# Kernel optimization log

Measured on AMD Instinct MI355X. Metric: run time of the kernel, lower is better.

## Reference

```python
import jax, jax.numpy as jnp
import numpy as np

BN_EPS = 1e-5

def _tok2img(f):
    # f: [197, 768] tokens (CLS first). Drop CLS, transpose, reshape -> [1, 768, 14, 14].
    # fv4[0, c, i, j] = f[1 + i*14 + j, c], identical to the original triple loop.
    return f[1:].T.reshape(1, 768, 14, 14)

def _resize(x, s):
    # PyTorch F.interpolate(mode='bilinear', align_corners=False) == jax.image.resize 'bilinear'
    n, c, h, w = x.shape
    return jax.image.resize(x, (n, c, h * s, w * s), method='bilinear')

def _conv_relu_bn(x, conv_w, conv_b, g, b, m, v):
    y = jax.lax.conv_general_dilated(x, conv_w, window_strides=(1, 1), padding='SAME',
                                     dimension_numbers=('NCHW', 'OIHW', 'NCHW'))
    y = y + conv_b[None, :, None, None]
    y = jax.nn.relu(y)
    # BatchNorm2d(1) in eval mode with running stats
    scale = g * jax.lax.rsqrt(v + BN_EPS)
    return y * scale[None, :, None, None] + (b - m * scale)[None, :, None, None]

def setup_inputs() -> dict:
    key = jax.random.key(0)
    ks = jax.random.split(key, 4)
    return {
        'x': jax.random.normal(ks[0], (14, 14), dtype=jnp.float32),
        'fv': jax.random.normal(ks[1], (4, 197, 768), dtype=jnp.float32),
        'conv_w': jax.random.normal(ks[2], (1, 769, 3, 3), dtype=jnp.float32) * 0.02,
        'conv_b': jnp.zeros((1,), jnp.float32),
        'bn_gamma': jnp.ones((1,), jnp.float32),
        'bn_beta': jnp.zeros((1,), jnp.float32),
        'bn_mean': jnp.zeros((1,), jnp.float32),
        'bn_var': jnp.ones((1,), jnp.float32),
        'W_w': jax.random.normal(ks[3], (224, 224), dtype=jnp.float32) * 0.05,
        'W_b': jnp.zeros((224,), jnp.float32),
    }

def reference(x, fv, conv_w, conv_b, bn_gamma, bn_beta, bn_mean, bn_var, W_w, W_b):
    h = x[None, None]  # [1,1,14,14]
    # skip features, pre-resized to match current resolution at each stage
    feats = (
        _tok2img(fv[3]),              # 14x14
        _resize(_tok2img(fv[2]), 2),  # 28x28
        _resize(_tok2img(fv[1]), 4),  # 56x56
        _resize(_tok2img(fv[0]), 8),  # 112x112
    )
    for f in feats:
        h = jnp.concatenate([h, f], axis=1)  # [1,769,H,W]
        h = _conv_relu_bn(h, conv_w, conv_b, bn_gamma, bn_beta, bn_mean, bn_var)
        h = _resize(h, 2)
    # Linear(224,224) over the last dim of [1,1,224,224]
    h = jnp.einsum('nchw,ow->ncho', h, W_w) + W_b
    return jax.nn.sigmoid(h)
```

## Files before the change

kernel.cpp:

```cpp
#include <hip/hip_runtime.h>
#include <math.h>


#define BN_EPS 1e-5f

__device__ __forceinline__ float clampf(float x, float lo, float hi) {
    return fminf(fmaxf(x, lo), hi);
}

__device__ __forceinline__ void srcRange(int dlo, int dhi, int srcH, int& slo, int& shi) {
    int H = 2 * srcH;
    int p0 = max(dlo - 1, 0), p1 = min(dhi + 1, H - 1);
    float h0 = fmaxf(((float)p0 + 0.5f) * 0.5f - 0.5f, 0.f);
    float h1 = fmaxf(((float)p1 + 0.5f) * 0.5f - 0.5f, 0.f);
    slo = (int)h0;
    shi = min((int)h1 + 1, srcH - 1);
}

__device__ __forceinline__ void bRange(int dlo, int dhi, int H, int& lo, int& hi) {
    float sc = 14.f / (float)H;
    int p0 = max(dlo - 1, 0), p1 = min(dhi + 1, H - 1);
    float f0 = clampf(((float)p0 + 0.5f) * sc - 0.5f, 0.f, 13.f);
    float f1 = clampf(((float)p1 + 0.5f) * sc - 0.5f, 0.f, 13.f);
    lo = (int)f0;
    hi = min((int)f1 + 1, 13);
}

__constant__ int kW[4] = {14, 28, 56, 112};
__constant__ int kG[4] = {0, 1764, 5292, 12348};

__global__ __launch_bounds__(1024)
void compute_B_kernel(const float* __restrict__ fv, const float* __restrict__ conv_w,
                      const float* __restrict__ W_w,
                      float* __restrict__ gBt, float* __restrict__ gWTf) {
    __shared__ float part[1008];
    __shared__ float sbrow[126];

    int b = blockIdx.x;
    int s = b / 14, u = b % 14;
    int tid = threadIdx.x;

    if (tid < 448) {
        int idx = b * 448 + tid;
        int o = idx % 224, xx = idx / 224;
        float acc = 0.f;
#pragma unroll
        for (int d = -1; d <= 2; ++d) {
            int w = 2 * xx + d;
            if (w < 0 || w > 223) continue;
            float hx = clampf(((float)w + 0.5f) * 0.5f - 0.5f, 0.f, 111.f);
            int xx0 = (int)hx; float fx = hx - (float)xx0; int xx1 = min(xx0 + 1, 111);
            float c = (xx0 == xx ? 1.f - fx : 0.f) + (xx1 == xx ? fx : 0.f);
            acc += c * W_w[o * 224 + w];
        }
        gWTf[xx * 224 + o] = acc;
    }

    if (tid < 1008) {
        int p = tid / 72, r = tid % 72;
        int sl = r / 9, t = r % 9;
        const float* fvrow = fv + ((size_t)(3 - s) * 197 + 1 + u * 14 + p) * 768 + sl * 96;
        const float* cwp = conv_w + (size_t)(1 + sl * 96) * 9 + t;
        float acc = 0.f;
#pragma unroll 32
        for (int m = 0; m < 96; ++m)
            acc += fvrow[m] * cwp[m * 9];
        part[(p * 9 + t) * 8 + sl] = acc;
    }
    __syncthreads();

    if (tid < 126) {
        float v = 0.f;
        int base = tid * 8;
#pragma unroll
        for (int k = 0; k < 8; ++k) v += part[base + k];
        sbrow[tid] = v;
    }
    __syncthreads();

    int W = kW[s], G = kG[s];
    int n = 9 * W;
    if (tid < n) {
        int t = tid / W, q = tid % W;
        float sc = 14.f / (float)W;
        float fx = clampf(((float)q + 0.5f) * sc - 0.5f, 0.f, 13.f);
        int x0 = (int)fx; float f = fx - (float)x0; int x1 = min(x0 + 1, 13);
        float val = (1.f - f) * sbrow[x0 * 9 + t] + f * sbrow[x1 * 9 + t];
        gBt[G + (t * 14 + u) * W + q] = val;
    }
}

__device__ __forceinline__ float stage_px(int i, int j, int H, int srcH,
                                          const float* __restrict__ hsrc, int srcLo,
                                          const float* __restrict__ cB, int nr, int bLo,
                                          const float* __restrict__ cw, float bias) {
    float featScale = 14.f / (float)H;
    float srcMax = (float)(srcH - 1);
    float acc = bias;
#pragma unroll
    for (int a = 0; a < 3; ++a) {
        int p = i + a - 1;
        if (p < 0 || p >= H) continue;
        float fy = clampf(((float)p + 0.5f) * featScale - 0.5f, 0.f, 13.f);
        int by0 = (int)fy; float byf = fy - (float)by0; int by1 = min(by0 + 1, 13);
        const float* b0 = cB + (by0 - bLo) * H;
        const float* b1 = cB + (by1 - bLo) * H;
        float hy = clampf(((float)p + 0.5f) * 0.5f - 0.5f, 0.f, srcMax);
        int hy0 = (int)hy; float fhy = hy - (float)hy0; int hy1 = min(hy0 + 1, srcH - 1);
        const float* h0 = hsrc + (hy0 - srcLo) * srcH;
        const float* h1 = hsrc + (hy1 - srcLo) * srcH;
#pragma unroll
        for (int bq = 0; bq < 3; ++bq) {
            int q = j + bq - 1;
            if (q < 0 || q >= H) continue;
            int t = a * 3 + bq;
            int toff = t * nr * H;
            float bv = (1.f - byf) * b0[toff + q] + byf * b1[toff + q];
            float hx = clampf(((float)q + 0.5f) * 0.5f - 0.5f, 0.f, srcMax);
            int hx0 = (int)hx; float fhx = hx - (float)hx0; int hx1 = min(hx0 + 1, srcH - 1);
            float hval = (1.f - fhy) * ((1.f - fhx) * h0[hx0] + fhx * h0[hx1])
                       + fhy         * ((1.f - fhx) * h1[hx0] + fhx * h1[hx1]);
            acc += cw[t] * hval + bv;
        }
    }
    return acc;
}

__global__ __launch_bounds__(1024, 1)
void refine_kernel(const float* __restrict__ x,
                   const float* __restrict__ conv_w, const float* __restrict__ conv_b,
                   const float* __restrict__ bng, const float* __restrict__ bnb,
                   const float* __restrict__ bnm, const float* __restrict__ bnv,
                   const float* __restrict__ W_b,
                   const float* __restrict__ gBt, const float* __restrict__ gWTf,
                   float* __restrict__ out) {
    __shared__ float cB0[9 * 9 * 14];
    __shared__ float cB1[9 * 7 * 28];
    __shared__ float cB2[9 * 5 * 56];
    __shared__ float cB3[9 * 4 * 112];
    __shared__ float y1w[9 * 14];
    __shared__ float y2w[7 * 28];
    __shared__ float y3w[6 * 56];
    __shared__ float y4loc[3 * 112];
    __shared__ float partial[12 * 224];

    int tid = threadIdx.x;
    int b = blockIdx.x;

    int y4lo = max(b - 1, 0), y4hi = min(b + 1, 111);
    int r3lo, r3hi; srcRange(y4lo, y4hi, 56, r3lo, r3hi);
    int r2lo, r2hi; srcRange(r3lo, r3hi, 28, r2lo, r2hi);
    int r1lo, r1hi; srcRange(r2lo, r2hi, 14, r1lo, r1hi);

    int bl0 = max(r1lo - 1, 0), bh0 = min(r1hi + 1, 13);
    int bl1, bh1; bRange(r2lo, r2hi, 28, bl1, bh1);
    int bl2, bh2; bRange(r3lo, r3hi, 56, bl2, bh2);
    int bl3, bh3; bRange(y4lo, y4hi, 112, bl3, bh3);
    int nr0 = min(bh0 - bl0 + 1, 9);
    int nr1 = min(bh1 - bl1 + 1, 7);
    int nr2 = min(bh2 - bl2 + 1, 5);
    int nr3 = min(bh3 - bl3 + 1, 4);

    {
        int m = nr0 * 14, n = 9 * m, base = kG[0] + bl0 * 14;
        for (int e = tid; e < n; e += 1024) { int t = e / m; cB0[e] = gBt[base + t * 196 + (e - t * m)]; }
    }
    {
        int m = nr1 * 28, n = 9 * m, base = kG[1] + bl1 * 28;
        for (int e = tid; e < n; e += 1024) { int t = e / m; cB1[e] = gBt[base + t * 392 + (e - t * m)]; }
    }
    {
        int m = nr2 * 56, n = 9 * m, base = kG[2] + bl2 * 56;
        for (int e = tid; e < n; e += 1024) { int t = e / m; cB2[e] = gBt[base + t * 784 + (e - t * m)]; }
    }
    {
        int m = nr3 * 112, n = 9 * m, base = kG[3] + bl3 * 112;
        for (int e = tid; e < n; e += 1024) { int t = e / m; cB3[e] = gBt[base + t * 1568 + (e - t * m)]; }
    }

    float cw[9];
#pragma unroll
    for (int t = 0; t < 9; ++t) cw[t] = conv_w[t];
    float bias = conv_b[0];
    float scale = bng[0] * rsqrtf(bnv[0] + BN_EPS);
    float shift = bnb[0] - bnm[0] * scale;
    __syncthreads();

    {
        int n = (r1hi - r1lo + 1) * 14;
        if (tid < n) {
            int i = r1lo + tid / 14, j = tid % 14;
            float acc = bias;
#pragma unroll
            for (int a = 0; a < 3; ++a) {
                int p = i + a - 1;
                if (p < 0 || p >= 14) continue;
#pragma unroll
                for (int bq = 0; bq < 3; ++bq) {
                    int q = j + bq - 1;
                    if (q < 0 || q >= 14) continue;
                    int t = a * 3 + bq;
                    acc += cw[t] * x[p * 14 + q] + cB0[(t * nr0 + (p - bl0)) * 14 + q];
                }
            }
            y1w[(i - r1lo) * 14 + j] = fmaxf(acc, 0.f) * scale + shift;
        }
    }
    __syncthreads();

    {
        int n = (r2hi - r2lo + 1) * 28;
        if (tid < n) {
            int i = r2lo + tid / 28, j = tid % 28;
            float acc = stage_px(i, j, 28, 14, y1w, r1lo, cB1, nr1, bl1, cw, bias);
            y2w[(i - r2lo) * 28 + j] = fmaxf(acc, 0.f) * scale + shift;
        }
    }
    __syncthreads();

    {
        int n = (r3hi - r3lo + 1) * 56;
        if (tid < n) {
            int i = r3lo + tid / 56, j = tid % 56;
            float acc = stage_px(i, j, 56, 28, y2w, r2lo, cB2, nr2, bl2, cw, bias);
            y3w[(i - r3lo) * 56 + j] = fmaxf(acc, 0.f) * scale + shift;
        }
    }
    __syncthreads();

    {
        int n = (y4hi - y4lo + 1) * 112;
        if (tid < n) {
            int i = y4lo + tid / 112, j = tid % 112;
            float acc = stage_px(i, j, 112, 56, y3w, r3lo, cB3, nr3, bl3, cw, bias);
            y4loc[(i - y4lo) * 112 + j] = fmaxf(acc, 0.f) * scale + shift;
        }
    }
    __syncthreads();

    if (tid < 896) {
        int kq = tid / 224, o = tid % 224;
        int k0 = kq * 28;
        float a0 = 0.f, a1 = 0.f, a2 = 0.f;
        for (int k = k0; k < k0 + 28; ++k) {
            float wf = gWTf[k * 224 + o];
            a0 += y4loc[k] * wf;
            a1 += y4loc[112 + k] * wf;
            a2 += y4loc[224 + k] * wf;
        }
        partial[(0 * 4 + kq) * 224 + o] = a0;
        partial[(1 * 4 + kq) * 224 + o] = a1;
        partial[(2 * 4 + kq) * 224 + o] = a2;
    }
    __syncthreads();

    if (tid < 448) {
        int rr = tid / 224, o = tid % 224;
        int r = 2 * b + rr;
        float hy = clampf(((float)r + 0.5f) * 0.5f - 0.5f, 0.f, 111.f);
        int yy0 = (int)hy; float fy = hy - (float)yy0; int yy1 = min(yy0 + 1, 111);
        int s0 = yy0 - y4lo, s1 = yy1 - y4lo;
        float D0 = partial[(s0 * 4 + 0) * 224 + o] + partial[(s0 * 4 + 1) * 224 + o]
                 + partial[(s0 * 4 + 2) * 224 + o] + partial[(s0 * 4 + 3) * 224 + o];
        float D1 = partial[(s1 * 4 + 0) * 224 + o] + partial[(s1 * 4 + 1) * 224 + o]
                 + partial[(s1 * 4 + 2) * 224 + o] + partial[(s1 * 4 + 3) * 224 + o];
        float v = (1.f - fy) * D0 + fy * D1 + W_b[o];
        out[(size_t)r * 224 + o] = 1.f / (1.f + expf(-v));
    }
}

extern "C" void kernel_launch(void* const* d_in, const int* in_sizes, int n_in,
                              void* d_out, int out_size, void* d_ws, size_t ws_size,
                              hipStream_t stream) {
    (void)in_sizes; (void)n_in; (void)out_size; (void)ws_size;
    const float* x      = (const float*)d_in[0];
    const float* fv     = (const float*)d_in[1];
    const float* conv_w = (const float*)d_in[2];
    const float* conv_b = (const float*)d_in[3];
    const float* bng    = (const float*)d_in[4];
    const float* bnb    = (const float*)d_in[5];
    const float* bnm    = (const float*)d_in[6];
    const float* bnv    = (const float*)d_in[7];
    const float* W_w    = (const float*)d_in[8];
    const float* W_b    = (const float*)d_in[9];
    float* out = (float*)d_out;

    float* ws   = (float*)d_ws;
    float* gBt  = ws;
    float* gWTf = ws + 26460;

    compute_B_kernel<<<56, 1024, 0, stream>>>(fv, conv_w, W_w, gBt, gWTf);
    refine_kernel<<<112, 1024, 0, stream>>>(x, conv_w, conv_b, bng, bnb, bnm, bnv,
                                            W_b, gBt, gWTf, out);
}
```

Measured before the change: 104.4 us.

## Stage conv weights in shared memory and use wavefront-per-row reductions in B kernel

The B kernel now stages the 768x9 conv weights (excluding the input-channel slice) into shared memory with a tap-major padded layout. Each wavefront then computes all nine tap dot products for one token row, reading the feature row coalesced and reducing with shuffles, which replaces the strided per-thread global loads and the shared partial-sum pass. The gWTf indexing is reorganised for coalesced access, and the per-stage cB gather loops drop integer division in favour of a fixed 9-tap loop. The cost is an extra ~27KB of shared memory per block and an added barrier.

```diff
diff --git a/kernel.cpp b/kernel.cpp
--- a/kernel.cpp
+++ b/kernel.cpp
@@ -33,16 +33,21 @@
 void compute_B_kernel(const float* __restrict__ fv, const float* __restrict__ conv_w,
                       const float* __restrict__ W_w,
                       float* __restrict__ gBt, float* __restrict__ gWTf) {
-    __shared__ float part[1008];
+    __shared__ float sWc[9 * 776];
     __shared__ float sbrow[126];
 
     int b = blockIdx.x;
     int s = b / 14, u = b % 14;
     int tid = threadIdx.x;
+    int wv = tid >> 6, lane = tid & 63;
+
+    for (int e = tid; e < 6912; e += 1024) {
+        int k = e / 9, t = e - k * 9;
+        sWc[t * 776 + k] = conv_w[9 + e];
+    }
 
     if (tid < 448) {
-        int idx = b * 448 + tid;
-        int o = idx % 224, xx = idx / 224;
+        int o = b * 4 + tid / 112, xx = tid % 112;
         float acc = 0.f;
 #pragma unroll
         for (int d = -1; d <= 2; ++d) {
@@ -55,33 +60,37 @@
         }
         gWTf[xx * 224 + o] = acc;
     }
-
-    if (tid < 1008) {
-        int p = tid / 72, r = tid % 72;
-        int sl = r / 9, t = r % 9;
-        const float* fvrow = fv + ((size_t)(3 - s) * 197 + 1 + u * 14 + p) * 768 + sl * 96;
-        const float* cwp = conv_w + (size_t)(1 + sl * 96) * 9 + t;
-        float acc = 0.f;
-#pragma unroll 32
-        for (int m = 0; m < 96; ++m)
-            acc += fvrow[m] * cwp[m * 9];
-        part[(p * 9 + t) * 8 + sl] = acc;
-    }
-    __syncthreads();
-
-    if (tid < 126) {
-        float v = 0.f;
-        int base = tid * 8;
-#pragma unroll
-        for (int k = 0; k < 8; ++k) v += part[base + k];
-        sbrow[tid] = v;
+    __syncthreads();
+
+    if (wv < 14) {
+        const float* fvrow = fv + ((size_t)(3 - s) * 197 + 1 + u * 14 + wv) * 768;
+        float acc[9];
+#pragma unroll
+        for (int t = 0; t < 9; ++t) acc[t] = 0.f;
+#pragma unroll 3
+        for (int m = 0; m < 12; ++m) {
+            float v = fvrow[lane + 64 * m];
+            const float* wp = sWc + lane + 64 * m;
+#pragma unroll
+            for (int t = 0; t < 9; ++t) acc[t] += v * wp[t * 776];
+        }
+#pragma unroll
+        for (int t = 0; t < 9; ++t) {
+#pragma unroll
+            for (int off = 32; off > 0; off >>= 1)
+                acc[t] += __shfl_down(acc[t], off, 64);
+        }
+        if (lane == 0) {
+#pragma unroll
+            for (int t = 0; t < 9; ++t) sbrow[wv * 9 + t] = acc[t];
+        }
     }
     __syncthreads();
 
     int W = kW[s], G = kG[s];
     int n = 9 * W;
     if (tid < n) {
-        int t = tid / W, q = tid % W;
+        int t = tid / W, q = tid - t * W;
         float sc = 14.f / (float)W;
         float fx = clampf(((float)q + 0.5f) * sc - 0.5f, 0.f, 13.f);
         int x0 = (int)fx; float f = fx - (float)x0; int x1 = min(x0 + 1, 13);
@@ -162,20 +171,28 @@
     int nr3 = min(bh3 - bl3 + 1, 4);
 
     {
-        int m = nr0 * 14, n = 9 * m, base = kG[0] + bl0 * 14;
-        for (int e = tid; e < n; e += 1024) { int t = e / m; cB0[e] = gBt[base + t * 196 + (e - t * m)]; }
-    }
-    {
-        int m = nr1 * 28, n = 9 * m, base = kG[1] + bl1 * 28;
-        for (int e = tid; e < n; e += 1024) { int t = e / m; cB1[e] = gBt[base + t * 392 + (e - t * m)]; }
-    }
-    {
-        int m = nr2 * 56, n = 9 * m, base = kG[2] + bl2 * 56;
-        for (int e = tid; e < n; e += 1024) { int t = e / m; cB2[e] = gBt[base + t * 784 + (e - t * m)]; }
-    }
-    {
-        int m = nr3 * 112, n = 9 * m, base = kG[3] + bl3 * 112;
-        for (int e = tid; e < n; e += 1024) { int t = e / m; cB3[e] = gBt[base + t * 1568 + (e - t * m)]; }
+        int m = nr0 * 14, base = kG[0] + bl0 * 14;
+#pragma unroll
+        for (int t = 0; t < 9; ++t)
+            if (tid < m) cB0[t * m + tid] = gBt[base + t * 196 + tid];
+    }
+    {
+        int m = nr1 * 28, base = kG[1] + bl1 * 28;
+#pragma unroll
+        for (int t = 0; t < 9; ++t)
+            if (tid < m) cB1[t * m + tid] = gBt[base + t * 392 + tid];
+    }
+    {
+        int m = nr2 * 56, base = kG[2] + bl2 * 56;
+#pragma unroll
+        for (int t = 0; t < 9; ++t)
+            if (tid < m) cB2[t * m + tid] = gBt[base + t * 784 + tid];
+    }
+    {
+        int m = nr3 * 112, base = kG[3] + bl3 * 112;
+#pragma unroll
+        for (int t = 0; t < 9; ++t)
+            if (tid < m) cB3[t * m + tid] = gBt[base + t * 1568 + tid];
     }
 
     float cw[9];
```

Result: faster. 87.53 us (-16.1%).
